# Kernel optimization log

Hardware: AMD Instinct MI355X
Metric: run time of the kernel (lower is better)

## Reference

```python
import jax, jax.numpy as jnp
import numpy as np

N_NODES = 100000


def _gcn_norm(edge_index, n):
    # PyG GCNConv default: add self-loops, symmetric normalization
    src, dst = edge_index[0], edge_index[1]
    loops = jnp.arange(n, dtype=src.dtype)
    src = jnp.concatenate([src, loops])
    dst = jnp.concatenate([dst, loops])
    deg = jax.ops.segment_sum(jnp.ones_like(dst, dtype=jnp.float32), dst, num_segments=n)
    dinv = jnp.where(deg > 0, jax.lax.rsqrt(deg), 0.0)
    norm = dinv[src] * dinv[dst]  # [E+N]
    return src, dst, norm


def _gcn_conv(x, src, dst, norm, W, b, n):
    h = x @ W                                  # [N, out] transform first
    msg = h[src] * norm[:, None]               # gather + edge weight
    out = jax.ops.segment_sum(msg, dst, num_segments=n)  # scatter-add
    return out + b


def setup_inputs() -> dict:
    key = jax.random.key(0)
    k1, k2, k3, k4 = jax.random.split(key, 4)
    in_f, h_f, out_f = 128, 256, 128
    x = jax.random.normal(k1, (N_NODES, in_f), dtype=jnp.float32)
    edge_index = jax.random.randint(k2, (2, 1600000), 0, N_NODES, dtype=jnp.int64)
    W1 = jax.random.normal(k3, (in_f, h_f), dtype=jnp.float32) / np.sqrt(in_f)
    b1 = jnp.zeros((h_f,), dtype=jnp.float32)
    W2 = jax.random.normal(k4, (h_f, out_f), dtype=jnp.float32) / np.sqrt(h_f)
    b2 = jnp.zeros((out_f,), dtype=jnp.float32)
    return {"x": x, "edge_index": edge_index, "W1": W1, "b1": b1, "W2": W2, "b2": b2}


def reference(x, edge_index, W1, b1, W2, b2):
    n = x.shape[0]
    src, dst, norm = _gcn_norm(edge_index, n)
    h = jax.nn.relu(_gcn_conv(x, src, dst, norm, W1, b1, n))
    return _gcn_conv(h, src, dst, norm, W2, b2, n)
```

## Files before the change

kernel.cpp:

```cpp
#include <hip/hip_runtime.h>

typedef __bf16 bf16x8 __attribute__((ext_vector_type(8)));
typedef float f32x4 __attribute__((ext_vector_type(4)));

#define DEVI static __device__ __forceinline__
#define CHUNK 8192

DEVI unsigned short f2bf(float f){
  unsigned int x = __builtin_bit_cast(unsigned int, f);
  x = (x + 0x7fffu + ((x >> 16) & 1u)) >> 16;
  return (unsigned short)x;
}
DEVI unsigned int packbf2(float a, float b){
  return (unsigned int)f2bf(a) | ((unsigned int)f2bf(b) << 16);
}
DEVI float bflo(unsigned int u){ return __builtin_bit_cast(float, u << 16); }
DEVI float bfhi(unsigned int u){ return __builtin_bit_cast(float, u & 0xffff0000u); }

__global__ void k_zero(int* __restrict__ p, int n){
  int i = blockIdx.x*256 + threadIdx.x;
  if (i < n) p[i] = 0;
}


__global__ __launch_bounds__(256) void kb_hist(const int* __restrict__ dst,
    int* __restrict__ bucketCnt, int E, int NB){
  __shared__ int h[2048];
  for (int i=threadIdx.x;i<NB;i+=256) h[i]=0;
  __syncthreads();
  int base = blockIdx.x*CHUNK;
  int lim = base+CHUNK < E ? base+CHUNK : E;
  for (int i = base+threadIdx.x; i < lim; i += 256)
    atomicAdd(&h[dst[i]>>8], 1);
  __syncthreads();
  for (int i=threadIdx.x;i<NB;i+=256)
    if (h[i]) atomicAdd(&bucketCnt[i], h[i]);
}

__global__ __launch_bounds__(256) void kb_scan(const int* __restrict__ bucketCnt,
    int* __restrict__ bucketOff, int* __restrict__ bucketCur, int NB){
  __shared__ int sh[256];
  int t = threadIdx.x;
  int per = (NB+255)/256;
  int vals[8];
  int lsum = 0;
  for (int j=0;j<per;j++){
    int i = t*per+j;
    int v = (i<NB) ? bucketCnt[i] : 0;
    vals[j]=v; lsum+=v;
  }
  sh[t]=lsum; __syncthreads();
  for (int off=1; off<256; off<<=1){
    int x = (t>=off) ? sh[t-off] : 0;
    __syncthreads();
    sh[t] += x;
    __syncthreads();
  }
  int run = sh[t]-lsum;
  for (int j=0;j<per;j++){
    int i = t*per+j;
    if (i<NB){ bucketOff[i]=run; bucketCur[i]=run; }
    run += vals[j];
  }
  if (t==255) bucketOff[NB]=run;
}

__global__ __launch_bounds__(256) void kb_scatter(const int* __restrict__ src,
    const int* __restrict__ dst, int* __restrict__ bucketCur,
    int* __restrict__ srcb, int* __restrict__ dstb, int E, int NB){
  __shared__ int h[2048];
  __shared__ int baseSh[2048];
  for (int i=threadIdx.x;i<NB;i+=256) h[i]=0;
  __syncthreads();
  int base = blockIdx.x*CHUNK;
  int lim = base+CHUNK < E ? base+CHUNK : E;
  for (int i = base+threadIdx.x; i < lim; i += 256)
    atomicAdd(&h[dst[i]>>8], 1);
  __syncthreads();
  for (int i=threadIdx.x;i<NB;i+=256){
    int c = h[i];
    baseSh[i] = c ? atomicAdd(&bucketCur[i], c) : 0;
    h[i] = 0;
  }
  __syncthreads();
  for (int i = base+threadIdx.x; i < lim; i += 256){
    int d = dst[i];
    int b = d>>8;
    int r = atomicAdd(&h[b], 1);
    int p = baseSh[b] + r;
    srcb[p] = src[i];
    dstb[p] = d;
  }
}

__global__ __launch_bounds__(256) void kb_cnt(const int* __restrict__ dstb,
    const int* __restrict__ bucketOff, int* __restrict__ cnt, int n){
  __shared__ int c[256];
  c[threadIdx.x]=0; __syncthreads();
  int b = blockIdx.x;
  int s = bucketOff[b], e2 = bucketOff[b+1];
  for (int i=s+threadIdx.x;i<e2;i+=256) atomicAdd(&c[dstb[i]&255], 1);
  __syncthreads();
  int node = b*256 + threadIdx.x;
  if (node < n) cnt[node] = c[threadIdx.x];
}

__global__ __launch_bounds__(256) void kb_fill(const int* __restrict__ srcb,
    const int* __restrict__ dstb, const int* __restrict__ bucketOff,
    const int* __restrict__ rp, int* __restrict__ csr){
  __shared__ int c[256];
  c[threadIdx.x]=0; __syncthreads();
  int b = blockIdx.x;
  int s = bucketOff[b], e2 = bucketOff[b+1];
  for (int i=s+threadIdx.x;i<e2;i+=256){
    int d = dstb[i];
    int r = atomicAdd(&c[d&255], 1);
    csr[rp[d]+r] = srcb[i];
  }
}


__global__ void k_scan1(const int* __restrict__ cnt, int* __restrict__ rp,
                        int* __restrict__ partials, int n){
  __shared__ int sh[256];
  int t = threadIdx.x;
  int base = blockIdx.x*1024 + t*4;
  int v0=0,v1=0,v2=0,v3=0;
  if (base+0 < n) v0 = cnt[base+0];
  if (base+1 < n) v1 = cnt[base+1];
  if (base+2 < n) v2 = cnt[base+2];
  if (base+3 < n) v3 = cnt[base+3];
  int s = v0+v1+v2+v3;
  sh[t] = s; __syncthreads();
  for (int off=1; off<256; off<<=1){
    int x = (t>=off) ? sh[t-off] : 0;
    __syncthreads();
    sh[t] += x;
    __syncthreads();
  }
  if (t==255) partials[blockIdx.x] = sh[255];
  int run = sh[t]-s;
  if (base+0 < n) rp[base+0] = run; run += v0;
  if (base+1 < n) rp[base+1] = run; run += v1;
  if (base+2 < n) rp[base+2] = run; run += v2;
  if (base+3 < n) rp[base+3] = run;
}

__global__ void k_scan2(int* __restrict__ partials, int P){
  __shared__ int sh[256];
  int t = threadIdx.x;
  int v = (t<P) ? partials[t] : 0;
  sh[t] = v; __syncthreads();
  for (int off=1; off<256; off<<=1){
    int x = (t>=off) ? sh[t-off] : 0;
    __syncthreads();
    sh[t] += x;
    __syncthreads();
  }
  if (t<P) partials[t] = sh[t]-v;
}

__global__ void k_scan3(int* __restrict__ rp, const int* __restrict__ partials,
                        int n, int E){
  int i = blockIdx.x*256 + threadIdx.x;
  if (i < n) rp[i] += partials[i>>10];
  else if (i == n) rp[n] = E;
}

__global__ void k_dinv(const int* __restrict__ cnt, float* __restrict__ dinv, int n){
  int i = blockIdx.x*256 + threadIdx.x;
  if (i<n) dinv[i] = rsqrtf((float)(cnt[i]+1));
}

__global__ void k_cvt(const float2* __restrict__ x, const float* __restrict__ dinv,
                      unsigned int* __restrict__ xb, int n2){
  int i = blockIdx.x*256 + threadIdx.x;
  if (i<n2){
    float d = dinv[i>>6];
    float2 v = x[i];
    xb[i] = packbf2(d*v.x, d*v.y);
  }
}

__global__ void k_pack(const float* __restrict__ W, unsigned short* __restrict__ Wp,
                       int N, int KS, int NF){
  int idx = blockIdx.x*256 + threadIdx.x;
  if (idx >= KS*NF*64) return;
  int l = idx & 63;
  int frag = idx >> 6;
  int cf = frag % NF;
  int ks = frag / NF;
  int kbase = ks*32 + (l>>4)*8;
  int col = cf*16 + (l&15);
  unsigned short* dp = Wp + (size_t)idx*8;
  for (int j=0;j<8;j++) dp[j] = f2bf(W[(size_t)(kbase+j)*N + col]);
}

template<bool FINAL>
__global__ __launch_bounds__(256) void k_agg(
    const unsigned int* __restrict__ xs, const int* __restrict__ rp,
    const int* __restrict__ csr, const float* __restrict__ dinv,
    const float* __restrict__ bias, unsigned int* __restrict__ outb,
    float* __restrict__ outf, int n){
  int node = blockIdx.x*4 + (threadIdx.x>>6);
  if (node >= n) return;
  int l = threadIdx.x & 63;
  float dn = dinv[node];
  unsigned int u = xs[(size_t)node*64 + l];
  float a0 = bflo(u), a1 = bfhi(u);
  int e = rp[node], end = rp[node+1];
  for (int base = e; base < end; base += 8){
    int idx[8];
    unsigned int v[8];
    #pragma unroll
    for (int i=0;i<8;i++){
      int ei = base+i < end-1 ? base+i : end-1;
      idx[i] = csr[ei];
    }
    #pragma unroll
    for (int i=0;i<8;i++)
      v[i] = xs[(size_t)idx[i]*64 + l];
    #pragma unroll
    for (int i=0;i<8;i++){
      if (base+i >= end) v[i] = 0;
      a0 += bflo(v[i]);
      a1 += bfhi(v[i]);
    }
  }
  if constexpr (FINAL){
    float2 r;
    r.x = a0*dn + bias[2*l];
    r.y = a1*dn + bias[2*l+1];
    *(float2*)(outf + (size_t)node*128 + 2*l) = r;
  } else {
    outb[(size_t)node*64 + l] = packbf2(a0*dn, a1*dn);
  }
}

template<int K, int N, bool BIASRELU, bool ROWSCALE>
__global__ __launch_bounds__(256) void k_gemm(
    const unsigned short* __restrict__ A, const unsigned short* __restrict__ Wp,
    const float* __restrict__ bias, const float* __restrict__ rowscale,
    unsigned short* __restrict__ C, int M){
  constexpr int KS = K/32;
  constexpr int NF = N/16;
  constexpr int NWC = N/64;
  constexpr int NWR = 4/NWC;
  constexpr int BM = 64*NWR;
  int l = threadIdx.x & 63;
  int w = threadIdx.x >> 6;
  int wr = w / NWC, wc = w % NWC;
  int r0 = blockIdx.x*BM + wr*64;
  int c0 = wc*64;
  int lr = l & 15, lg = l >> 4;
  f32x4 acc[4][4];
  #pragma unroll
  for (int i=0;i<4;i++)
    #pragma unroll
    for (int j=0;j<4;j++)
      acc[i][j] = f32x4{0.f,0.f,0.f,0.f};
  for (int ks=0; ks<KS; ++ks){
    bf16x8 a[4], b[4];
    #pragma unroll
    for (int ar=0;ar<4;ar++){
      int row = r0 + ar*16 + lr;
      if (row > M-1) row = M-1;
      const uint4* p = (const uint4*)(A + (size_t)row*K + ks*32 + lg*8);
      union { uint4 u; bf16x8 v; } t; t.u = *p; a[ar] = t.v;
    }
    #pragma unroll
    for (int cb=0;cb<4;cb++){
      int cf = (c0>>4) + cb;
      const uint4* p = (const uint4*)(Wp + ((size_t)(ks*NF + cf)*64 + l)*8);
      union { uint4 u; bf16x8 v; } t; t.u = *p; b[cb] = t.v;
    }
    #pragma unroll
    for (int ar=0;ar<4;ar++)
      #pragma unroll
      for (int cb=0;cb<4;cb++)
        acc[ar][cb] = __builtin_amdgcn_mfma_f32_16x16x32_bf16(a[ar], b[cb], acc[ar][cb], 0, 0, 0);
  }
  #pragma unroll
  for (int ar=0;ar<4;ar++){
    #pragma unroll
    for (int i=0;i<4;i++){
      int row = r0 + ar*16 + lg*4 + i;
      if (row < M){
        float rs = 1.f;
        if constexpr (ROWSCALE) rs = rowscale[row];
        #pragma unroll
        for (int cb=0;cb<4;cb++){
          int col = c0 + cb*16 + lr;
          float v = acc[ar][cb][i];
          if constexpr (BIASRELU){ v += bias[col]; v = fmaxf(v, 0.f); }
          if constexpr (ROWSCALE) v *= rs;
          C[(size_t)row*N + col] = f2bf(v);
        }
      }
    }
  }
}

extern "C" void kernel_launch(void* const* d_in, const int* in_sizes, int n_in,
                              void* d_out, int out_size, void* d_ws, size_t ws_size,
                              hipStream_t stream){
  const float* x  = (const float*)d_in[0];
  const int*   ei = (const int*)d_in[1];
  const float* W1 = (const float*)d_in[2];
  const float* b1 = (const float*)d_in[3];
  const float* W2 = (const float*)d_in[4];
  const float* b2 = (const float*)d_in[5];
  const int IN_F = 128, H_F = 256, OUT_F = 128;
  int n = in_sizes[0] / IN_F;
  int E = in_sizes[1] / 2;
  const int* srcI = ei;
  const int* dstI = ei + E;
  const int NB = (n+255)>>8;

  char* ws = (char*)d_ws;
  size_t off = 0;
  auto alloc = [&](size_t bytes)->char*{
    char* p = ws + off; off += (bytes + 255) & ~(size_t)255; return p;
  };
  int*   cnt   = (int*)  alloc((size_t)n*4);
  int*   rp    = (int*)  alloc(((size_t)n+1)*4);
  float* dinv  = (float*)alloc((size_t)n*4);
  int*   parts = (int*)  alloc(1024);
  int*   bCnt  = (int*)  alloc((size_t)NB*4);
  int*   bOff  = (int*)  alloc(((size_t)NB+1)*4);
  int*   bCur  = (int*)  alloc((size_t)NB*4);
  unsigned short* W1p = (unsigned short*)alloc((size_t)IN_F*H_F*2);
  unsigned short* W2p = (unsigned short*)alloc((size_t)H_F*OUT_F*2);
  int*   csr   = (int*)  alloc((size_t)E*4);
  unsigned int* xb = (unsigned int*)alloc((size_t)n*(IN_F/2)*4);
  unsigned int* AX = (unsigned int*)alloc((size_t)n*(IN_F/2)*4);
  unsigned short* H1 = (unsigned short*)alloc((size_t)n*H_F*2);
  int* srcb = (int*)H1;
  int* dstb = srcb + E;

  int g256n = (n+255)/256;
  int P = (n+1023)/1024;
  int NCH = (E + CHUNK - 1)/CHUNK;

  k_zero<<<(NB+255)/256,256,0,stream>>>(bCnt, NB);
  kb_hist<<<NCH,256,0,stream>>>(dstI, bCnt, E, NB);
  kb_scan<<<1,256,0,stream>>>(bCnt, bOff, bCur, NB);
  kb_scatter<<<NCH,256,0,stream>>>(srcI, dstI, bCur, srcb, dstb, E, NB);
  kb_cnt<<<NB,256,0,stream>>>(dstb, bOff, cnt, n);
  k_scan1<<<P,256,0,stream>>>(cnt, rp, parts, n);
  k_scan2<<<1,256,0,stream>>>(parts, P);
  k_scan3<<<(n+256)/256,256,0,stream>>>(rp, parts, n, E);
  k_dinv<<<g256n,256,0,stream>>>(cnt, dinv, n);
  k_cvt<<<((n*(IN_F/2))+255)/256,256,0,stream>>>((const float2*)x, dinv, xb, n*(IN_F/2));
  k_pack<<<16,256,0,stream>>>(W1, W1p, H_F, IN_F/32, H_F/16);
  k_pack<<<16,256,0,stream>>>(W2, W2p, OUT_F, H_F/32, OUT_F/16);
  kb_fill<<<NB,256,0,stream>>>(srcb, dstb, bOff, rp, csr);
  k_agg<false><<<(n+3)/4,256,0,stream>>>(xb, rp, csr, dinv, nullptr, AX, nullptr, n);
  k_gemm<128,256,true,false><<<(n+63)/64,256,0,stream>>>((const unsigned short*)AX, W1p, b1, nullptr, H1, n);
  unsigned int* T = xb;
  k_gemm<256,128,false,true><<<(n+127)/128,256,0,stream>>>(H1, W2p, nullptr, dinv, (unsigned short*)T, n);
  k_agg<true><<<(n+3)/4,256,0,stream>>>(T, rp, csr, dinv, b2, nullptr, (float*)d_out, n);
}
```

Before: 287.8 us.

## Fuse CSR count/scan/fill into one kernel and vectorize aggregation gathers

```diff
diff --git a/kernel.cpp b/kernel.cpp
--- a/kernel.cpp
+++ b/kernel.cpp
@@ -4,7 +4,7 @@
 typedef float f32x4 __attribute__((ext_vector_type(4)));
 
 #define DEVI static __device__ __forceinline__
-#define CHUNK 8192
+#define CHUNK 4096
 
 DEVI unsigned short f2bf(float f){
   unsigned int x = __builtin_bit_cast(unsigned int, f);
@@ -93,83 +93,41 @@
   }
 }
 
-__global__ __launch_bounds__(256) void kb_cnt(const int* __restrict__ dstb,
-    const int* __restrict__ bucketOff, int* __restrict__ cnt, int n){
+__global__ __launch_bounds__(256) void kb_fused(const int* __restrict__ srcb,
+    const int* __restrict__ dstb, const int* __restrict__ bOff,
+    int* __restrict__ rp, int* __restrict__ csr, float* __restrict__ dinv,
+    int n, int NB, int E){
   __shared__ int c[256];
-  c[threadIdx.x]=0; __syncthreads();
+  __shared__ int sh[256];
+  __shared__ int cur[256];
+  int t = threadIdx.x;
   int b = blockIdx.x;
-  int s = bucketOff[b], e2 = bucketOff[b+1];
-  for (int i=s+threadIdx.x;i<e2;i+=256) atomicAdd(&c[dstb[i]&255], 1);
-  __syncthreads();
-  int node = b*256 + threadIdx.x;
-  if (node < n) cnt[node] = c[threadIdx.x];
-}
-
-__global__ __launch_bounds__(256) void kb_fill(const int* __restrict__ srcb,
-    const int* __restrict__ dstb, const int* __restrict__ bucketOff,
-    const int* __restrict__ rp, int* __restrict__ csr){
-  __shared__ int c[256];
-  c[threadIdx.x]=0; __syncthreads();
-  int b = blockIdx.x;
-  int s = bucketOff[b], e2 = bucketOff[b+1];
-  for (int i=s+threadIdx.x;i<e2;i+=256){
-    int d = dstb[i];
-    int r = atomicAdd(&c[d&255], 1);
-    csr[rp[d]+r] = srcb[i];
-  }
-}
-
-
-__global__ void k_scan1(const int* __restrict__ cnt, int* __restrict__ rp,
-                        int* __restrict__ partials, int n){
-  __shared__ int sh[256];
-  int t = threadIdx.x;
-  int base = blockIdx.x*1024 + t*4;
-  int v0=0,v1=0,v2=0,v3=0;
-  if (base+0 < n) v0 = cnt[base+0];
-  if (base+1 < n) v1 = cnt[base+1];
-  if (base+2 < n) v2 = cnt[base+2];
-  if (base+3 < n) v3 = cnt[base+3];
-  int s = v0+v1+v2+v3;
-  sh[t] = s; __syncthreads();
-  for (int off=1; off<256; off<<=1){
-    int x = (t>=off) ? sh[t-off] : 0;
+  int s = bOff[b], e2 = bOff[b+1];
+  c[t]=0; __syncthreads();
+  for (int i=s+t;i<e2;i+=256) atomicAdd(&c[dstb[i]&255], 1);
+  __syncthreads();
+  int deg = c[t];
+  sh[t]=deg; __syncthreads();
+  for (int o=1;o<256;o<<=1){
+    int x = (t>=o) ? sh[t-o] : 0;
     __syncthreads();
-    sh[t] += x;
+    sh[t]+=x;
     __syncthreads();
   }
-  if (t==255) partials[blockIdx.x] = sh[255];
-  int run = sh[t]-s;
-  if (base+0 < n) rp[base+0] = run; run += v0;
-  if (base+1 < n) rp[base+1] = run; run += v1;
-  if (base+2 < n) rp[base+2] = run; run += v2;
-  if (base+3 < n) rp[base+3] = run;
-}
-
-__global__ void k_scan2(int* __restrict__ partials, int P){
-  __shared__ int sh[256];
-  int t = threadIdx.x;
-  int v = (t<P) ? partials[t] : 0;
-  sh[t] = v; __syncthreads();
-  for (int off=1; off<256; off<<=1){
-    int x = (t>=off) ? sh[t-off] : 0;
-    __syncthreads();
-    sh[t] += x;
-    __syncthreads();
-  }
-  if (t<P) partials[t] = sh[t]-v;
-}
-
-__global__ void k_scan3(int* __restrict__ rp, const int* __restrict__ partials,
-                        int n, int E){
-  int i = blockIdx.x*256 + threadIdx.x;
-  if (i < n) rp[i] += partials[i>>10];
-  else if (i == n) rp[n] = E;
-}
-
-__global__ void k_dinv(const int* __restrict__ cnt, float* __restrict__ dinv, int n){
-  int i = blockIdx.x*256 + threadIdx.x;
-  if (i<n) dinv[i] = rsqrtf((float)(cnt[i]+1));
+  int excl = sh[t]-deg;
+  int node = b*256+t;
+  if (node<n){
+    rp[node] = s + excl;
+    dinv[node] = rsqrtf((float)(deg+1));
+  }
+  if (b==NB-1 && t==0) rp[n] = E;
+  cur[t] = s + excl;
+  __syncthreads();
+  for (int i=s+t;i<e2;i+=256){
+    int d = dstb[i]&255;
+    int r = atomicAdd(&cur[d], 1);
+    csr[r] = srcb[i] << 8;
+  }
 }
 
 __global__ void k_cvt(const float2* __restrict__ x, const float* __restrict__ dinv,
@@ -182,10 +140,8 @@
   }
 }
 
-__global__ void k_pack(const float* __restrict__ W, unsigned short* __restrict__ Wp,
-                       int N, int KS, int NF){
-  int idx = blockIdx.x*256 + threadIdx.x;
-  if (idx >= KS*NF*64) return;
+DEVI void packW(const float* __restrict__ W, unsigned short* __restrict__ Wp,
+                int idx, int N, int NF){
   int l = idx & 63;
   int frag = idx >> 6;
   int cf = frag % NF;
@@ -193,8 +149,19 @@
   int kbase = ks*32 + (l>>4)*8;
   int col = cf*16 + (l&15);
   unsigned short* dp = Wp + (size_t)idx*8;
+  #pragma unroll
   for (int j=0;j<8;j++) dp[j] = f2bf(W[(size_t)(kbase+j)*N + col]);
 }
+
+__global__ void k_pack2(const float* __restrict__ W1, unsigned short* __restrict__ W1p,
+                        const float* __restrict__ W2, unsigned short* __restrict__ W2p){
+  int idx = blockIdx.x*256 + threadIdx.x;
+  if (idx < 4096) packW(W1, W1p, idx, 256, 16);
+  else            packW(W2, W2p, idx-4096, 128, 8);
+}
+
+#define ACC8(V) { a0+=bflo(V.x); a1+=bfhi(V.x); a2+=bflo(V.y); a3+=bfhi(V.y); \
+                  a4+=bflo(V.z); a5+=bfhi(V.z); a6+=bflo(V.w); a7+=bfhi(V.w); }
 
 template<bool FINAL>
 __global__ __launch_bounds__(256) void k_agg(
@@ -205,35 +172,76 @@
   int node = blockIdx.x*4 + (threadIdx.x>>6);
   if (node >= n) return;
   int l = threadIdx.x & 63;
+  int q = l & 15;
+  int h = l >> 4;
+  const char* xbase = (const char*)xs;
+  float a0=0,a1=0,a2=0,a3=0,a4=0,a5=0,a6=0,a7=0;
+  int e = rp[node], end = rp[node+1];
+  int p = e;
+  int nf = (end - e) >> 4;
+  for (int blk=0; blk<nf; ++blk, p+=16){
+    uint4 v[4];
+    #pragma unroll
+    for (int i=0;i<4;i++){
+      int boff = csr[p + 4*i + h];
+      v[i] = *(const uint4*)(xbase + (size_t)(unsigned)boff + q*16);
+    }
+    ACC8(v[0]); ACC8(v[1]); ACC8(v[2]); ACC8(v[3]);
+  }
+  int rem = end - p;
+  if (rem >= 8){
+    uint4 v[2];
+    #pragma unroll
+    for (int i=0;i<2;i++){
+      int boff = csr[p + 4*i + h];
+      v[i] = *(const uint4*)(xbase + (size_t)(unsigned)boff + q*16);
+    }
+    ACC8(v[0]); ACC8(v[1]);
+    p += 8; rem -= 8;
+  }
+  if (rem > 0){
+    uint4 v[2];
+    #pragma unroll
+    for (int i=0;i<2;i++){
+      int ei = p + 4*i + h;
+      int ec = ei < end-1 ? ei : end-1;
+      int boff = csr[ec];
+      uint4 t = *(const uint4*)(xbase + (size_t)(unsigned)boff + q*16);
+      if (ei >= end){ t.x=0; t.y=0; t.z=0; t.w=0; }
+      v[i] = t;
+    }
+    ACC8(v[0]); ACC8(v[1]);
+  }
+  a0 += __shfl_xor(a0,16); a0 += __shfl_xor(a0,32);
+  a1 += __shfl_xor(a1,16); a1 += __shfl_xor(a1,32);
+  a2 += __shfl_xor(a2,16); a2 += __shfl_xor(a2,32);
+  a3 += __shfl_xor(a3,16); a3 += __shfl_xor(a3,32);
+  a4 += __shfl_xor(a4,16); a4 += __shfl_xor(a4,32);
+  a5 += __shfl_xor(a5,16); a5 += __shfl_xor(a5,32);
+  a6 += __shfl_xor(a6,16); a6 += __shfl_xor(a6,32);
+  a7 += __shfl_xor(a7,16); a7 += __shfl_xor(a7,32);
+  uint4 sv = *(const uint4*)(xbase + (size_t)node*256 + q*16);
+  ACC8(sv);
   float dn = dinv[node];
-  unsigned int u = xs[(size_t)node*64 + l];
-  float a0 = bflo(u), a1 = bfhi(u);
-  int e = rp[node], end = rp[node+1];
-  for (int base = e; base < end; base += 8){
-    int idx[8];
-    unsigned int v[8];
-    #pragma unroll
-    for (int i=0;i<8;i++){
-      int ei = base+i < end-1 ? base+i : end-1;
-      idx[i] = csr[ei];
-    }
-    #pragma unroll
-    for (int i=0;i<8;i++)
-      v[i] = xs[(size_t)idx[i]*64 + l];
-    #pragma unroll
-    for (int i=0;i<8;i++){
-      if (base+i >= end) v[i] = 0;
-      a0 += bflo(v[i]);
-      a1 += bfhi(v[i]);
-    }
-  }
   if constexpr (FINAL){
-    float2 r;
-    r.x = a0*dn + bias[2*l];
-    r.y = a1*dn + bias[2*l+1];
-    *(float2*)(outf + (size_t)node*128 + 2*l) = r;
+    if (h < 2){
+      const float4 bb = *(const float4*)(bias + 8*q + 4*h);
+      float4 r;
+      r.x = (h ? a4 : a0)*dn + bb.x;
+      r.y = (h ? a5 : a1)*dn + bb.y;
+      r.z = (h ? a6 : a2)*dn + bb.z;
+      r.w = (h ? a7 : a3)*dn + bb.w;
+      *(float4*)(outf + (size_t)node*128 + 8*q + 4*h) = r;
+    }
   } else {
-    outb[(size_t)node*64 + l] = packbf2(a0*dn, a1*dn);
+    if (h == 0){
+      uint4 o;
+      o.x = packbf2(a0*dn, a1*dn);
+      o.y = packbf2(a2*dn, a3*dn);
+      o.z = packbf2(a4*dn, a5*dn);
+      o.w = packbf2(a6*dn, a7*dn);
+      *(uint4*)((char*)outb + (size_t)node*256 + q*16) = o;
+    }
   }
 }
 
@@ -322,10 +330,8 @@
   auto alloc = [&](size_t bytes)->char*{
     char* p = ws + off; off += (bytes + 255) & ~(size_t)255; return p;
   };
-  int*   cnt   = (int*)  alloc((size_t)n*4);
   int*   rp    = (int*)  alloc(((size_t)n+1)*4);
   float* dinv  = (float*)alloc((size_t)n*4);
-  int*   parts = (int*)  alloc(1024);
   int*   bCnt  = (int*)  alloc((size_t)NB*4);
   int*   bOff  = (int*)  alloc(((size_t)NB+1)*4);
   int*   bCur  = (int*)  alloc((size_t)NB*4);
@@ -338,23 +344,15 @@
   int* srcb = (int*)H1;
   int* dstb = srcb + E;
 
-  int g256n = (n+255)/256;
-  int P = (n+1023)/1024;
   int NCH = (E + CHUNK - 1)/CHUNK;
 
   k_zero<<<(NB+255)/256,256,0,stream>>>(bCnt, NB);
   kb_hist<<<NCH,256,0,stream>>>(dstI, bCnt, E, NB);
   kb_scan<<<1,256,0,stream>>>(bCnt, bOff, bCur, NB);
   kb_scatter<<<NCH,256,0,stream>>>(srcI, dstI, bCur, srcb, dstb, E, NB);
-  kb_cnt<<<NB,256,0,stream>>>(dstb, bOff, cnt, n);
-  k_scan1<<<P,256,0,stream>>>(cnt, rp, parts, n);
-  k_scan2<<<1,256,0,stream>>>(parts, P);
-  k_scan3<<<(n+256)/256,256,0,stream>>>(rp, parts, n, E);
-  k_dinv<<<g256n,256,0,stream>>>(cnt, dinv, n);
+  kb_fused<<<NB,256,0,stream>>>(srcb, dstb, bOff, rp, csr, dinv, n, NB, E);
   k_cvt<<<((n*(IN_F/2))+255)/256,256,0,stream>>>((const float2*)x, dinv, xb, n*(IN_F/2));
-  k_pack<<<16,256,0,stream>>>(W1, W1p, H_F, IN_F/32, H_F/16);
-  k_pack<<<16,256,0,stream>>>(W2, W2p, OUT_F, H_F/32, OUT_F/16);
-  kb_fill<<<NB,256,0,stream>>>(srcb, dstb, bOff, rp, csr);
+  k_pack2<<<32,256,0,stream>>>(W1, W1p, W2, W2p);
   k_agg<false><<<(n+3)/4,256,0,stream>>>(xb, rp, csr, dinv, nullptr, AX, nullptr, n);
   k_gemm<128,256,true,false><<<(n+63)/64,256,0,stream>>>((const unsigned short*)AX, W1p, b1, nullptr, H1, n);
   unsigned int* T = xb;
```

Result: faster. 282.1 us (-2.0%).
